# Optimization experiments

Hardware: AMD Instinct MI355X
Metric: run time of the kernel (lower is better)

Reference implementation:

```python
import jax, jax.numpy as jnp
import numpy as np

B, V = 128, 128000


def setup_inputs() -> dict:
    key = jax.random.key(0)
    k1, k2, k3, k4, k5, k6 = jax.random.split(key, 6)
    logits = jax.random.normal(k1, (B, V), dtype=jnp.float32)
    temperatures = jax.random.uniform(k2, (B,), dtype=jnp.float32, minval=0.5, maxval=1.5)
    top_ks = jax.random.randint(k3, (B,), 1, 2049).astype(jnp.int64)
    top_ps = jax.random.uniform(k4, (B,), dtype=jnp.float32, minval=0.8, maxval=1.0)
    min_ps = jax.random.uniform(k5, (B,), dtype=jnp.float32, minval=0.0, maxval=0.1)
    u = jax.random.uniform(k6, (B,), dtype=jnp.float32)
    return {"logits": logits, "temperatures": temperatures, "top_ks": top_ks,
            "top_ps": top_ps, "min_ps": min_ps, "u": u}


def reference(logits, temperatures, top_ks, top_ps, min_ps, u):
    # temperature-scaled softmax
    probs = jax.nn.softmax(logits.astype(jnp.float32) / temperatures[:, None], axis=-1)  # [B,V]

    # --- top_k_renorm_prob: keep k largest probs per row, renormalize ---
    sorted_desc = jnp.sort(probs, axis=-1)[:, ::-1]  # [B,V] descending
    k_idx = jnp.clip(top_ks - 1, 0, probs.shape[-1] - 1).astype(jnp.int32)[:, None]
    k_thresh = jnp.take_along_axis(sorted_desc, k_idx, axis=-1)  # [B,1] k-th largest prob
    probs = jnp.where(probs >= k_thresh, probs, 0.0)
    probs = probs / jnp.sum(probs, axis=-1, keepdims=True)

    # --- top_p_renorm_prob: keep smallest prefix of sorted probs covering mass p ---
    sorted_desc = jnp.sort(probs, axis=-1)[:, ::-1]
    cum = jnp.cumsum(sorted_desc, axis=-1)
    keep_sorted = (cum - sorted_desc) < top_ps[:, None]  # always keeps at least the top token
    p_thresh = jnp.min(jnp.where(keep_sorted, sorted_desc, jnp.inf), axis=-1, keepdims=True)
    probs = jnp.where(probs >= p_thresh, probs, 0.0)
    probs = probs / jnp.sum(probs, axis=-1, keepdims=True)

    # --- min_p_sampling_from_probs: drop probs < min_p * max_prob, renorm, sample ---
    max_p = jnp.max(probs, axis=-1, keepdims=True)
    probs = jnp.where(probs >= min_ps[:, None] * max_p, probs, 0.0)
    probs = probs / jnp.sum(probs, axis=-1, keepdims=True)

    # inverse-CDF (multinomial) sampling with per-row uniform u
    cdf = jnp.cumsum(probs, axis=-1)
    tokens = jnp.sum(cdf < u[:, None], axis=-1)
    tokens = jnp.clip(tokens, 0, probs.shape[-1] - 1).astype(jnp.int32)
    return tokens
```

## Files before the change

### kernel.cpp

```cpp
#include <hip/hip_runtime.h>
#include <float.h>
#include <stdint.h>

#define TPB_H 1024
#define TPB_G 1024
#define TPB_S 512
#define NB 2048
#define NS 4
#define CAND_CAP 2048
#define KEPT_CAP 4096
#define MAXLEV 6
#define NW_H (TPB_H / 64)
#define NW_S (TPB_S / 64)
#define FLO (-16.0f)
#define FSC ((float)NB / 32.0f)

__device__ __forceinline__ int bin_of(float x, float lo, float sc) {
  float bf = (x - lo) * sc;
  if (!(bf > 0.0f)) return 0;
  if (bf >= (float)(NB - 1)) return NB - 1;
  return (int)bf;
}

__device__ __forceinline__ double wsum_d(double v) {
#pragma unroll
  for (int o = 32; o > 0; o >>= 1) v += __shfl_xor(v, o);
  return v;
}
__device__ __forceinline__ int wsum_i(int v) {
#pragma unroll
  for (int o = 32; o > 0; o >>= 1) v += __shfl_xor(v, o);
  return v;
}
__device__ __forceinline__ float wmax_f(float v) {
#pragma unroll
  for (int o = 32; o > 0; o >>= 1) v = fmaxf(v, __shfl_xor(v, o));
  return v;
}

__device__ __forceinline__ int wave_push(int* cnt_lds, bool active) {
  const unsigned long long mask = __ballot(active);
  if (mask == 0ull) return -1;
  const int lane = (int)(threadIdx.x & 63);
  const unsigned long long lanebit = 1ull << lane;
  const int prefix = __popcll(mask & (lanebit - 1ull));
  const int leader = (int)(__ffsll((unsigned long long)mask) - 1);
  int base = 0;
  if (active && prefix == 0) base = atomicAdd(cnt_lds, __popcll(mask));
  base = __shfl(base, leader);
  return base + prefix;
}

__device__ __forceinline__ double blk_sum_d(double v, double* sred, double* out) {
  v = wsum_d(v);
  __syncthreads();
  if ((threadIdx.x & 63) == 0) sred[threadIdx.x >> 6] = v;
  __syncthreads();
  if (threadIdx.x == 0) {
    double t = 0.0;
#pragma unroll
    for (int i = 0; i < NW_S; i++) t += sred[i];
    *out = t;
  }
  __syncthreads();
  return *out;
}

__device__ __forceinline__ int blk_sum_i(int v, int* sredi, int* out) {
  v = wsum_i(v);
  __syncthreads();
  if ((threadIdx.x & 63) == 0) sredi[threadIdx.x >> 6] = v;
  __syncthreads();
  if (threadIdx.x == 0) {
    int t = 0;
#pragma unroll
    for (int i = 0; i < NW_S; i++) t += sredi[i];
    *out = t;
  }
  __syncthreads();
  return *out;
}

__device__ __forceinline__ double blk_exscan_d(double v, double* sw, double* sw2) {
  const int tid = threadIdx.x;
  const int lane = tid & 63, wid = tid >> 6;
  __syncthreads();
  double incl = v;
#pragma unroll
  for (int o = 1; o < 64; o <<= 1) {
    double t = __shfl_up(incl, o);
    if (lane >= o) incl += t;
  }
  if (lane == 63) sw[wid] = incl;
  __syncthreads();
  if (tid == 0) {
    double acc = 0.0;
#pragma unroll
    for (int i = 0; i < NW_S; i++) { double t = sw[i]; sw2[i] = acc; acc += t; }
  }
  __syncthreads();
  return sw2[wid] + (incl - v);
}


__device__ __forceinline__ void xchg_f(float& k, int& p, int e, int s, int len) {
  const float ok = __shfl_xor(k, s);
  const int op = __shfl_xor(p, s);
  const bool lower = ((e & s) == 0);
  const bool desc = (((e & ~s) & len) == 0);
  const bool keep = desc ? (lower ? (k >= ok) : (k <= ok))
                         : (lower ? (k <= ok) : (k >= ok));
  if (!keep) { k = ok; p = op; }
}

__device__ __forceinline__ void xchg_i(int& k, float& p, int e, int s, int len) {
  const int ok = __shfl_xor(k, s);
  const float op = __shfl_xor(p, s);
  const bool lower = ((e & s) == 0);
  const bool asc = (((e & ~s) & len) == 0);
  const bool keep = asc ? (lower ? (k <= ok) : (k >= ok))
                        : (lower ? (k >= ok) : (k <= ok));
  if (!keep) { k = ok; p = op; }
}

__device__ __forceinline__ void reg_sort128_f(float& ka, int& pa, float& kb, int& pb,
                                              int base, int lane) {
  const int ea = base + lane, eb = base + 64 + lane;
  for (int len = 2; len <= 128; len <<= 1) {
    if (len == 128) {
      const bool d = ((base & 128) == 0);
      if (d ? (ka < kb) : (ka > kb)) {
        float tk = ka; ka = kb; kb = tk; int tp = pa; pa = pb; pb = tp;
      }
      for (int s = 32; s >= 1; s >>= 1) { xchg_f(ka, pa, ea, s, len); xchg_f(kb, pb, eb, s, len); }
    } else {
      for (int s = len >> 1; s >= 1; s >>= 1) { xchg_f(ka, pa, ea, s, len); xchg_f(kb, pb, eb, s, len); }
    }
  }
}

__device__ __forceinline__ void reg_merge128_f(float& ka, int& pa, float& kb, int& pb,
                                               int base, int lane, int len) {
  const int ea = base + lane, eb = base + 64 + lane;
  const bool d = ((base & len) == 0);
  if (d ? (ka < kb) : (ka > kb)) {
    float tk = ka; ka = kb; kb = tk; int tp = pa; pa = pb; pb = tp;
  }
  for (int s = 32; s >= 1; s >>= 1) { xchg_f(ka, pa, ea, s, len); xchg_f(kb, pb, eb, s, len); }
}

__device__ __forceinline__ void reg_sort128_i(int& ka, float& pa, int& kb, float& pb,
                                              int base, int lane) {
  const int ea = base + lane, eb = base + 64 + lane;
  for (int len = 2; len <= 128; len <<= 1) {
    if (len == 128) {
      const bool a = ((base & 128) == 0);
      if (a ? (ka > kb) : (ka < kb)) {
        int tk = ka; ka = kb; kb = tk; float tp = pa; pa = pb; pb = tp;
      }
      for (int s = 32; s >= 1; s >>= 1) { xchg_i(ka, pa, ea, s, len); xchg_i(kb, pb, eb, s, len); }
    } else {
      for (int s = len >> 1; s >= 1; s >>= 1) { xchg_i(ka, pa, ea, s, len); xchg_i(kb, pb, eb, s, len); }
    }
  }
}

__device__ __forceinline__ void reg_merge128_i(int& ka, float& pa, int& kb, float& pb,
                                               int base, int lane, int len) {
  const int ea = base + lane, eb = base + 64 + lane;
  const bool a = ((base & len) == 0);
  if (a ? (ka > kb) : (ka < kb)) {
    int tk = ka; ka = kb; kb = tk; float tp = pa; pa = pb; pb = tp;
  }
  for (int s = 32; s >= 1; s >>= 1) { xchg_i(ka, pa, ea, s, len); xchg_i(kb, pb, eb, s, len); }
}

__device__ void bitonic_desc_f(float* key, int* pay, int M) {
  const int tid = threadIdx.x;
  for (int len = 2; len <= M; len <<= 1) {
    for (int str = len >> 1; str > 0; str >>= 1) {
      for (int t = tid; t < (M >> 1); t += TPB_S) {
        const int i = ((t & ~(str - 1)) << 1) | (t & (str - 1));
        const int j2 = i | str;
        const float vi = key[i], vj = key[j2];
        const bool descSeg = ((i & len) == 0);
        if (descSeg ? (vi < vj) : (vi > vj)) {
          key[i] = vj; key[j2] = vi;
          const int ti = pay[i]; pay[i] = pay[j2]; pay[j2] = ti;
        }
      }
      __syncthreads();
    }
  }
}

__device__ void bitonic_asc_i(int* key, float* pay, int M) {
  const int tid = threadIdx.x;
  for (int len = 2; len <= M; len <<= 1) {
    for (int str = len >> 1; str > 0; str >>= 1) {
      for (int t = tid; t < (M >> 1); t += TPB_S) {
        const int i = ((t & ~(str - 1)) << 1) | (t & (str - 1));
        const int j2 = i | str;
        const int ki = key[i], kj = key[j2];
        const bool ascSeg = ((i & len) == 0);
        if (ascSeg ? (ki > kj) : (ki < kj)) {
          key[i] = kj; key[j2] = ki;
          const float tv = pay[i]; pay[i] = pay[j2]; pay[j2] = tv;
        }
      }
      __syncthreads();
    }
  }
}

__device__ void hybrid_sort_desc_f(float* key, int* pay, int M) {
  const int tid = threadIdx.x;
  const int wid = tid >> 6, lane = tid & 63;
  const int nblk = M >> 7;
  __syncthreads();
  for (int blk = wid; blk < nblk; blk += NW_S) {
    const int base = blk << 7;
    float ka = key[base + lane]; int pa = pay[base + lane];
    float kb = key[base + 64 + lane]; int pb = pay[base + 64 + lane];
    reg_sort128_f(ka, pa, kb, pb, base, lane);
    key[base + lane] = ka; pay[base + lane] = pa;
    key[base + 64 + lane] = kb; pay[base + 64 + lane] = pb;
  }
  __syncthreads();
  for (int len = 256; len <= M; len <<= 1) {
    for (int str = len >> 1; str >= 128; str >>= 1) {
      for (int t = tid; t < (M >> 1); t += TPB_S) {
        const int i = ((t & ~(str - 1)) << 1) | (t & (str - 1));
        const int j2 = i | str;
        const float vi = key[i], vj = key[j2];
        const bool d = ((i & len) == 0);
        if (d ? (vi < vj) : (vi > vj)) {
          key[i] = vj; key[j2] = vi;
          const int ti = pay[i]; pay[i] = pay[j2]; pay[j2] = ti;
        }
      }
      __syncthreads();
    }
    for (int blk = wid; blk < nblk; blk += NW_S) {
      const int base = blk << 7;
      float ka = key[base + lane]; int pa = pay[base + lane];
      float kb = key[base + 64 + lane]; int pb = pay[base + 64 + lane];
      reg_merge128_f(ka, pa, kb, pb, base, lane, len);
      key[base + lane] = ka; pay[base + lane] = pa;
      key[base + 64 + lane] = kb; pay[base + 64 + lane] = pb;
    }
    __syncthreads();
  }
}

__device__ void hybrid_sort_asc_i(int* key, float* pay, int M) {
  const int tid = threadIdx.x;
  const int wid = tid >> 6, lane = tid & 63;
  const int nblk = M >> 7;
  __syncthreads();
  for (int blk = wid; blk < nblk; blk += NW_S) {
    const int base = blk << 7;
    int ka = key[base + lane]; float pa = pay[base + lane];
    int kb = key[base + 64 + lane]; float pb = pay[base + 64 + lane];
    reg_sort128_i(ka, pa, kb, pb, base, lane);
    key[base + lane] = ka; pay[base + lane] = pa;
    key[base + 64 + lane] = kb; pay[base + 64 + lane] = pb;
  }
  __syncthreads();
  for (int len = 256; len <= M; len <<= 1) {
    for (int str = len >> 1; str >= 128; str >>= 1) {
      for (int t = tid; t < (M >> 1); t += TPB_S) {
        const int i = ((t & ~(str - 1)) << 1) | (t & (str - 1));
        const int j2 = i | str;
        const int ki = key[i], kj = key[j2];
        const bool a = ((i & len) == 0);
        if (a ? (ki > kj) : (ki < kj)) {
          key[i] = kj; key[j2] = ki;
          const float tv = pay[i]; pay[i] = pay[j2]; pay[j2] = tv;
        }
      }
      __syncthreads();
    }
    for (int blk = wid; blk < nblk; blk += NW_S) {
      const int base = blk << 7;
      int ka = key[base + lane]; float pa = pay[base + lane];
      int kb = key[base + 64 + lane]; float pb = pay[base + 64 + lane];
      reg_merge128_i(ka, pa, kb, pb, base, lane, len);
      key[base + lane] = ka; pay[base + lane] = pa;
      key[base + 64 + lane] = kb; pay[base + 64 + lane] = pb;
    }
    __syncthreads();
  }
}

__device__ __forceinline__ void locate_kbin(const int* hist, int k,
                                            int* s_bin, int* s_kk, int* s_cntbin) {
  if (threadIdx.x < 64) {
    const int l = threadIdx.x;
    const int b0 = NB - (l + 1) * (NB / 64);
    int c = 0;
#pragma unroll
    for (int j = 0; j < NB / 64; j++) c += hist[b0 + j];
    int incl = c;
#pragma unroll
    for (int o = 1; o < 64; o <<= 1) {
      int t2 = __shfl_up(incl, o);
      if (l >= o) incl += t2;
    }
    const int pref = incl - c;
    if (pref < k && k <= pref + c) {
      int rem = k - pref;
      for (int j = NB / 64 - 1; j >= 0; j--) {
        const int h = hist[b0 + j];
        if (rem <= h) { *s_bin = b0 + j; *s_cntbin = h; *s_kk = rem; break; }
        rem -= h;
      }
    }
  }
}

__device__ __forceinline__ int decode_k(const void* topks_raw, int row, int B, int V) {
  const int* ip = (const int*)topks_raw;
  const bool is64 = (B < 2) || (ip[1] == 0);
  long long kraw = is64 ? ((const long long*)topks_raw)[row] : (long long)ip[row];
  long long kidx = kraw - 1;
  if (kidx < 0) kidx = 0;
  if (kidx > (long long)(V - 1)) kidx = (long long)(V - 1);
  return (int)kidx + 1;
}

#define ROW_LOOP(...)                                                                  \
  do {                                                                                 \
    for (int i0_ = tid * 4; i0_ < V4; i0_ += TPB_S * 4) {                              \
      const float4 v4_ = *reinterpret_cast<const float4*>(lr + i0_);                   \
      { const float lv = v4_.x; const int gi = i0_ + 0; (void)gi; __VA_ARGS__ }        \
      { const float lv = v4_.y; const int gi = i0_ + 1; (void)gi; __VA_ARGS__ }        \
      { const float lv = v4_.z; const int gi = i0_ + 2; (void)gi; __VA_ARGS__ }        \
      { const float lv = v4_.w; const int gi = i0_ + 3; (void)gi; __VA_ARGS__ }        \
    }                                                                                  \
    for (int gi = V4 + tid; gi < V; gi += TPB_S) {                                     \
      const float lv = lr[gi]; (void)gi; __VA_ARGS__                                   \
    }                                                                                  \
  } while (0)

extern "C" __global__ void __launch_bounds__(TPB_H) hist_max_kernel(
    const float* __restrict__ logits, int V,
    int* __restrict__ ws_hist, float* __restrict__ ws_max,
    int* __restrict__ kept_cnt, int* __restrict__ cand_cnt, int zeroCnts) {
  __shared__ int hist[NB];
  __shared__ float sredf[NW_H];
  const int tid = threadIdx.x;
  const int row = blockIdx.x / NS;
  const int part = blockIdx.x % NS;
  const float* lr = logits + (size_t)row * (size_t)V;
  const int start = (int)(((long long)V * part) / NS);
  const int end = (int)(((long long)V * (part + 1)) / NS);
  const int cnt = end - start;

  if (zeroCnts && part == 0 && tid == 0) { kept_cnt[row] = 0; cand_cnt[row] = 0; }

  for (int i = tid; i < NB; i += TPB_H) hist[i] = 0;
  __syncthreads();

  float mx = -FLT_MAX;
  const int c4 = ((start & 3) == 0) ? (cnt & ~3) : 0;
  for (int i0 = tid * 4; i0 < c4; i0 += TPB_H * 4) {
    const float4 v4 = *reinterpret_cast<const float4*>(lr + start + i0);
    mx = fmaxf(mx, v4.x); atomicAdd(&hist[bin_of(v4.x, FLO, FSC)], 1);
    mx = fmaxf(mx, v4.y); atomicAdd(&hist[bin_of(v4.y, FLO, FSC)], 1);
    mx = fmaxf(mx, v4.z); atomicAdd(&hist[bin_of(v4.z, FLO, FSC)], 1);
    mx = fmaxf(mx, v4.w); atomicAdd(&hist[bin_of(v4.w, FLO, FSC)], 1);
  }
  for (int i = c4 + tid; i < cnt; i += TPB_H) {
    const float lv = lr[start + i];
    mx = fmaxf(mx, lv); atomicAdd(&hist[bin_of(lv, FLO, FSC)], 1);
  }

  mx = wmax_f(mx);
  __syncthreads();
  if ((tid & 63) == 0) sredf[tid >> 6] = mx;
  __syncthreads();
  if (tid == 0) {
    float t = sredf[0];
    for (int i = 1; i < NW_H; i++) t = fmaxf(t, sredf[i]);
    ws_max[blockIdx.x] = t;
  }
  __syncthreads();
  int* dst = ws_hist + (size_t)blockIdx.x * NB;
  for (int i = tid; i < NB; i += TPB_H) dst[i] = hist[i];
}

extern "C" __global__ void __launch_bounds__(TPB_G) gather_kernel(
    const float* __restrict__ logits, const void* __restrict__ topks_raw,
    int V, int B, const int* __restrict__ ws_hist,
    int* __restrict__ kept_cnt, int* __restrict__ cand_cnt,
    float* __restrict__ kept_val_g, int* __restrict__ kept_idx_g,
    float* __restrict__ cand_val_g, int* __restrict__ cand_idx_g) {
  __shared__ int hist[NB];
  __shared__ float lkv[KEPT_CAP];
  __shared__ int lki[KEPT_CAP];
  __shared__ float lcv[CAND_CAP];
  __shared__ int lci[CAND_CAP];
  __shared__ int s_bin, s_kk, s_cntbin, l_kc, l_cc, s_gk, s_gc;
  const int tid = threadIdx.x;
  const int row = blockIdx.x / NS;
  const int part = blockIdx.x % NS;
  const int k = decode_k(topks_raw, row, B, V);

  for (int i = tid; i < NB; i += TPB_G) {
    int t = 0;
#pragma unroll
    for (int p = 0; p < NS; p++) t += ws_hist[(size_t)(row * NS + p) * NB + i];
    hist[i] = t;
  }
  if (tid == 0) { l_kc = 0; l_cc = 0; }
  __syncthreads();
  locate_kbin(hist, k, &s_bin, &s_kk, &s_cntbin);
  __syncthreads();
  const int kbin = s_bin;

  const float* lr = logits + (size_t)row * (size_t)V;
  const int start = (int)(((long long)V * part) / NS);
  const int end = (int)(((long long)V * (part + 1)) / NS);
  const int cnt = end - start;

#define GATHER_ONE(lv, gi)                                                   \
  {                                                                          \
    const int b_ = bin_of(lv, FLO, FSC);                                     \
    const bool isk_ = (b_ > kbin);                                           \
    const bool isc_ = (b_ == kbin);                                          \
    const int pk_ = wave_push(&l_kc, isk_);                                  \
    if (isk_ && pk_ < KEPT_CAP) { lkv[pk_] = lv; lki[pk_] = gi; }            \
    const int pc_ = wave_push(&l_cc, isc_);                                  \
    if (isc_ && pc_ < CAND_CAP) { lcv[pc_] = lv; lci[pc_] = gi; }            \
  }

  const int c4 = ((start & 3) == 0) ? (cnt & ~3) : 0;
  for (int i0 = tid * 4; i0 < c4; i0 += TPB_G * 4) {
    const float4 v4 = *reinterpret_cast<const float4*>(lr + start + i0);
    GATHER_ONE(v4.x, start + i0 + 0);
    GATHER_ONE(v4.y, start + i0 + 1);
    GATHER_ONE(v4.z, start + i0 + 2);
    GATHER_ONE(v4.w, start + i0 + 3);
  }
  for (int i = c4 + tid; i < cnt; i += TPB_G) {
    const float lv = lr[start + i];
    GATHER_ONE(lv, start + i);
  }
#undef GATHER_ONE

  __syncthreads();
  if (tid == 0) {
    s_gk = atomicAdd(&kept_cnt[row], l_kc);
    s_gc = atomicAdd(&cand_cnt[row], l_cc);
  }
  __syncthreads();
  {
    float* kv = kept_val_g + (size_t)row * KEPT_CAP;
    int* ki = kept_idx_g + (size_t)row * KEPT_CAP;
    float* cv = cand_val_g + (size_t)row * CAND_CAP;
    int* ci = cand_idx_g + (size_t)row * CAND_CAP;
    const int nks = (l_kc < KEPT_CAP) ? l_kc : KEPT_CAP;
    const int ncs = (l_cc < CAND_CAP) ? l_cc : CAND_CAP;
    for (int t = tid; t < nks; t += TPB_G) {
      const int d = s_gk + t;
      if (d < KEPT_CAP) { kv[d] = lkv[t]; ki[d] = lki[t]; }
    }
    for (int t = tid; t < ncs; t += TPB_G) {
      const int d = s_gc + t;
      if (d < CAND_CAP) { cv[d] = lcv[t]; ci[d] = lci[t]; }
    }
  }
}

extern "C" __global__ void __launch_bounds__(TPB_S) sampler_kernel(
    const float* __restrict__ logits, const float* __restrict__ temps,
    const void* __restrict__ topks_raw, const float* __restrict__ topps,
    const float* __restrict__ minps, const float* __restrict__ uarr,
    int* __restrict__ out, const int* __restrict__ ws_hist,
    const float* __restrict__ ws_max, const int* __restrict__ kept_cnt,
    const int* __restrict__ cand_cnt, const float* __restrict__ kept_val_g,
    const int* __restrict__ kept_idx_g, const float* __restrict__ cand_val_g,
    const int* __restrict__ cand_idx_g, int mode, int V, int B) {
  const int row = blockIdx.x;
  const int tid = threadIdx.x;

  __shared__ float cand[CAND_CAP];
  __shared__ int hist[NB];
  __shared__ int cand_idx[CAND_CAP];
  __shared__ int kept_idx[KEPT_CAP];
  __shared__ float kept_val[KEPT_CAP];
  __shared__ double sred[NW_S], sred2[NW_S];
  __shared__ int sredi[NW_S];
  __shared__ float sredf[NW_S];
  __shared__ double s_outd;
  __shared__ int s_outi;
  __shared__ int s_bad;
  __shared__ float lev_lo[MAXLEV], lev_sc[MAXLEV];
  __shared__ int lev_bin[MAXLEV];
  __shared__ int s_nlev, s_bin, s_kk, s_cntbin, s_cnt, s_ccnt, s_pos;
  __shared__ float s_lmax, s_vkl, s_lo, s_sc;

  const float* lr = logits + (size_t)row * (size_t)V;
  const float T = temps[row];
  const float topp = topps[row];
  const float minp = minps[row];
  const float u = uarr[row];
  const int k = decode_k(topks_raw, row, B, V);
  const int V4 = ((V & 3) == 0) ? V : 0;
  const int haveWs = (mode >= 1) ? 1 : 0;

  int n1 = -1;
  float lmax = 0.0f;

  if (mode == 2) {
    const int nk = kept_cnt[row];
    const int nc = cand_cnt[row];
    const int kk0 = k - nk;
    if (nk <= KEPT_CAP && nc >= 1 && nc <= CAND_CAP && kk0 >= 1 && kk0 <= nc) {
      if (tid == 0) {
        float m = ws_max[row * NS];
#pragma unroll
        for (int p = 1; p < NS; p++) m = fmaxf(m, ws_max[row * NS + p]);
        s_lmax = m;
      }
      for (int t = tid; t < nc; t += TPB_S) {
        cand[t] = cand_val_g[(size_t)row * CAND_CAP + t];
        cand_idx[t] = cand_idx_g[(size_t)row * CAND_CAP + t];
      }
      __syncthreads();
      for (int t = tid; t < nc; t += TPB_S) {
        const float v = cand[t];
        int rank = 0;
        for (int j = 0; j < nc; j++) {
          const float cj = cand[j];
          rank += (cj > v) ? 1 : ((cj == v && j < t) ? 1 : 0);
        }
        if (rank == kk0 - 1) s_vkl = v;
      }
      __syncthreads();
      const float vkl = s_vkl;
      for (int t = tid; t < nk; t += TPB_S) {
        kept_val[t] = kept_val_g[(size_t)row * KEPT_CAP + t];
        kept_idx[t] = kept_idx_g[(size_t)row * KEPT_CAP + t];
      }
      if (tid == 0) s_cnt = nk;
      __syncthreads();
      for (int t = tid; t < nc; t += TPB_S) {
        const float v = cand[t];
        if (v >= vkl) {
          const int p = atomicAdd(&s_cnt, 1);
          if (p < KEPT_CAP) { kept_val[p] = v; kept_idx[p] = cand_idx[t]; }
        }
      }
      __syncthreads();
      n1 = (s_cnt < KEPT_CAP) ? s_cnt : KEPT_CAP;
      lmax = s_lmax;
    }
  }

  if (n1 < 0) {
    if (haveWs) {
      for (int i = tid; i < NB; i += TPB_S) {
        int t = 0;
#pragma unroll
        for (int p = 0; p < NS; p++) t += ws_hist[(size_t)(row * NS + p) * NB + i];
        hist[i] = t;
      }
      if (tid == 0) {
        float m = ws_max[row * NS];
#pragma unroll
        for (int p = 1; p < NS; p++) m = fmaxf(m, ws_max[row * NS + p]);
        s_lmax = m;
      }
      __syncthreads();
    } else {
      for (int i = tid; i < NB; i += TPB_S) hist[i] = 0;
      __syncthreads();
      float mx = -FLT_MAX;
      ROW_LOOP(mx = fmaxf(mx, lv); atomicAdd(&hist[bin_of(lv, FLO, FSC)], 1););
      mx = wmax_f(mx);
      __syncthreads();
      if ((tid & 63) == 0) sredf[tid >> 6] = mx;
      __syncthreads();
      if (tid == 0) {
        float t = sredf[0];
        for (int i = 1; i < NW_S; i++) t = fmaxf(t, sredf[i]);
        s_lmax = t;
      }
      __syncthreads();
    }
    lmax = s_lmax;

    if (tid == 0) {
      s_kk = k; s_nlev = 0; s_vkl = lmax; s_lo = FLO; s_sc = FSC;
    }
    __syncthreads();

    for (int lev = 0; lev < MAXLEV; lev++) {
      if (tid < 64) {
        const int l = tid;
        const int b0 = NB - (l + 1) * (NB / 64);
        int c = 0;
#pragma unroll
        for (int j = 0; j < NB / 64; j++) c += hist[b0 + j];
        int incl = c;
#pragma unroll
        for (int o = 1; o < 64; o <<= 1) {
          int t2 = __shfl_up(incl, o);
          if (l >= o) incl += t2;
        }
        const int pref = incl - c;
        const int kk = s_kk;
        if (pref < kk && kk <= pref + c) {
          int rem = kk - pref;
          for (int j = NB / 64 - 1; j >= 0; j--) {
            const int h = hist[b0 + j];
            if (rem <= h) { s_bin = b0 + j; s_cntbin = h; s_kk = rem; break; }
            rem -= h;
          }
        }
      }
      __syncthreads();
      if (tid == 0) {
        lev_lo[lev] = s_lo; lev_sc[lev] = s_sc; lev_bin[lev] = s_bin;
        s_nlev = lev + 1;
      }
      __syncthreads();
      if (s_cntbin <= CAND_CAP) break;
      const float nlo = s_lo + (float)s_bin / s_sc;
      const float nsc = s_sc * (float)NB;
      const bool degw = !((nlo + (float)NB / nsc) > nlo);
      if (lev + 1 >= MAXLEV || degw) break;
      __syncthreads();
      if (tid == 0) { s_lo = nlo; s_sc = nsc; }
      for (int i = tid; i < NB; i += TPB_S) hist[i] = 0;
      __syncthreads();
      const int nl = lev + 1;
      ROW_LOOP(
        bool memb = true;
        for (int L = 0; L < nl; L++) {
          if (bin_of(lv, lev_lo[L], lev_sc[L]) != lev_bin[L]) { memb = false; break; }
        }
        if (memb) atomicAdd(&hist[bin_of(lv, nlo, nsc)], 1););
      __syncthreads();
    }

    if (tid == 0) { s_cnt = 0; s_ccnt = 0; }
    __syncthreads();
    {
      const int nl = s_nlev;
      ROW_LOOP(
        int cls = 2;
        for (int L = 0; L < nl; L++) {
          const int b = bin_of(lv, lev_lo[L], lev_sc[L]);
          if (b > lev_bin[L]) { cls = 1; break; }
          if (b < lev_bin[L]) { cls = 0; break; }
        }
        if (cls == 1) {
          int p = atomicAdd(&s_cnt, 1);
          if (p < KEPT_CAP) { kept_idx[p] = gi; kept_val[p] = lv; }
        } else if (cls == 2) {
          int p = atomicAdd(&s_ccnt, 1);
          if (p < CAND_CAP) { cand[p] = lv; cand_idx[p] = gi; }
        });
    }
    __syncthreads();

    {
      const int n = (s_ccnt < CAND_CAP) ? s_ccnt : CAND_CAP;
      int kkq = s_kk;
      if (kkq > n) kkq = n;
      for (int t = tid; t < n; t += TPB_S) {
        const float v = cand[t];
        int rank = 0;
        for (int j = 0; j < n; j++) {
          const float cj = cand[j];
          rank += (cj > v) ? 1 : ((cj == v && j < t) ? 1 : 0);
        }
        if (rank == kkq - 1) s_vkl = v;
      }
    }
    __syncthreads();
    const float vkl = s_vkl;
    {
      const int n = (s_ccnt < CAND_CAP) ? s_ccnt : CAND_CAP;
      for (int t = tid; t < n; t += TPB_S) {
        const float v = cand[t];
        if (v >= vkl) {
          int p = atomicAdd(&s_cnt, 1);
          if (p < KEPT_CAP) { kept_idx[p] = cand_idx[t]; kept_val[p] = v; }
        }
      }
    }
    __syncthreads();
    n1 = (s_cnt < KEPT_CAP) ? s_cnt : KEPT_CAP;
  }

  if (n1 <= 0) {
    if (tid == 0) out[row] = 0;
    return;
  }

  const float xmaxT = lmax / T;
  double lsum = 0.0;
  for (int t = tid; t < n1; t += TPB_S) {
    const float x = kept_val[t] / T;
    const float w = expf(x - xmaxT);
    kept_val[t] = w;
    lsum += (double)w;
  }
  const float s1f = (float)blk_sum_d(lsum, sred, &s_outd);
  for (int t = tid; t < n1; t += TPB_S) kept_val[t] = kept_val[t] / s1f;

  int M = 128;
  while (M < n1) M <<= 1;
  __syncthreads();
  for (int t = n1 + tid; t < M; t += TPB_S) { kept_val[t] = -1.0f; kept_idx[t] = 0x7FFFFFFF; }
  __syncthreads();
  hybrid_sort_desc_f(kept_val, kept_idx, M);
  if (tid == 0) s_bad = 0;
  __syncthreads();
  for (int t = tid; t + 1 < M; t += TPB_S)
    if (kept_val[t] < kept_val[t + 1]) s_bad = 1;
  __syncthreads();
  if (s_bad) bitonic_desc_f(kept_val, kept_idx, M);

  const int C = (M + TPB_S - 1) / TPB_S;
  double cls0 = 0.0;
  for (int j = 0; j < C; j++) {
    const int p = tid * C + j;
    if (p < n1) cls0 += (double)kept_val[p];
  }
  const double excl0 = blk_exscan_d(cls0, sred, sred2);
  int lc = 0;
  {
    double run = excl0;
    for (int j = 0; j < C; j++) {
      const int p = tid * C + j;
      if (p < n1) {
        if (run < (double)topp) lc++;
        run += (double)kept_val[p];
      }
    }
  }
  const int cnt = blk_sum_i(lc, sredi, &s_outi);
  const float pthr = kept_val[cnt - 1];

  int ln2 = 0;
  double ls2 = 0.0;
  for (int j = 0; j < C; j++) {
    const int p = tid * C + j;
    if (p < n1) {
      const float v = kept_val[p];
      if (v >= pthr) { ln2++; ls2 += (double)v; }
    }
  }
  const int n2 = blk_sum_i(ln2, sredi, &s_outi);
  const float s2f = (float)blk_sum_d(ls2, sred, &s_outd);

  const float maxr = kept_val[0] / s2f;
  const float th4 = minp * maxr;
  int ln3 = 0;
  double ls3 = 0.0;
  for (int j = 0; j < C; j++) {
    const int p = tid * C + j;
    if (p < n2) {
      const float r = kept_val[p] / s2f;
      if (r >= th4) { ln3++; ls3 += (double)r; }
    }
  }
  const int n3 = blk_sum_i(ln3, sredi, &s_outi);
  const float s3f = (float)blk_sum_d(ls3, sred, &s_outd);

  int M3 = 128;
  while (M3 < n3) M3 <<= 1;
  __syncthreads();
  for (int t = tid; t < M3; t += TPB_S) {
    if (t < n3) {
      const float r = kept_val[t] / s2f;
      kept_val[t] = r / s3f;
    } else {
      kept_val[t] = 0.0f;
      kept_idx[t] = 0x7FFFFFFF;
    }
  }
  __syncthreads();
  hybrid_sort_asc_i(kept_idx, kept_val, M3);
  if (tid == 0) s_bad = 0;
  __syncthreads();
  for (int t = tid; t + 1 < M3; t += TPB_S)
    if (kept_idx[t] > kept_idx[t + 1]) s_bad = 1;
  __syncthreads();
  if (s_bad) bitonic_asc_i(kept_idx, kept_val, M3);

  const int C3 = (M3 + TPB_S - 1) / TPB_S;
  double cls3 = 0.0;
  for (int j = 0; j < C3; j++) {
    const int p = tid * C3 + j;
    if (p < n3) cls3 += (double)kept_val[p];
  }
  const double e5 = blk_exscan_d(cls3, sred, sred2);
  if (tid == 0) s_pos = 0x7FFFFFFF;
  __syncthreads();
  {
    double run = e5;
    int found = -1;
    for (int j = 0; j < C3; j++) {
      const int p = tid * C3 + j;
      if (p < n3) {
        run += (double)kept_val[p];
        if (run >= (double)u) { found = p; break; }
      }
    }
    if (found >= 0) atomicMin(&s_pos, found);
  }
  __syncthreads();
  if (tid == 0) {
    int token;
    if (!(u > 0.0f)) token = 0;
    else if (s_pos == 0x7FFFFFFF) token = V - 1;
    else token = kept_idx[s_pos];
    out[row] = token;
  }
}

extern "C" void kernel_launch(void* const* d_in, const int* in_sizes, int n_in,
                              void* d_out, int out_size, void* d_ws, size_t ws_size,
                              hipStream_t stream) {
  const float* logits = (const float*)d_in[0];
  const float* temps = (const float*)d_in[1];
  const void* topks = d_in[2];
  const float* topps = (const float*)d_in[3];
  const float* minps = (const float*)d_in[4];
  const float* u = (const float*)d_in[5];
  int* out = (int*)d_out;
  const int B = in_sizes[1];
  const int V = in_sizes[0] / B;
  (void)n_in; (void)out_size;

  char* p = (char*)d_ws;
  int* ws_hist = (int*)p;        p += (size_t)NS * B * NB * sizeof(int);
  float* ws_max = (float*)p;     p += (size_t)NS * B * sizeof(float);
  int* kept_cnt = (int*)p;       p += (size_t)B * sizeof(int);
  int* cand_cnt = (int*)p;       p += (size_t)B * sizeof(int);
  float* kept_val_g = (float*)p; p += (size_t)B * KEPT_CAP * sizeof(float);
  int* kept_idx_g = (int*)p;     p += (size_t)B * KEPT_CAP * sizeof(int);
  float* cand_val_g = (float*)p; p += (size_t)B * CAND_CAP * sizeof(float);
  int* cand_idx_g = (int*)p;     p += (size_t)B * CAND_CAP * sizeof(int);
  const size_t need_full = (size_t)(p - (char*)d_ws);
  const size_t need_hist = (size_t)NS * B * NB * sizeof(int) + (size_t)NS * B * sizeof(float);

  int mode = 0;
  if (d_ws && ws_size >= need_full) mode = 2;
  else if (d_ws && ws_size >= need_hist) mode = 1;

  if (mode >= 1) {
    hist_max_kernel<<<dim3(B * NS), dim3(TPB_H), 0, stream>>>(
        logits, V, ws_hist, ws_max, kept_cnt, cand_cnt, (mode == 2) ? 1 : 0);
  }
  if (mode == 2) {
    gather_kernel<<<dim3(B * NS), dim3(TPB_G), 0, stream>>>(
        logits, topks, V, B, ws_hist, kept_cnt, cand_cnt,
        kept_val_g, kept_idx_g, cand_val_g, cand_idx_g);
  }
  sampler_kernel<<<dim3(B), dim3(TPB_S), 0, stream>>>(
      logits, temps, topks, topps, minps, u, out, ws_hist, ws_max,
      kept_cnt, cand_cnt, kept_val_g, kept_idx_g, cand_val_g, cand_idx_g,
      mode, V, B);
}
```

Before: 200.9 us.

## Use 512-element register bitonic sorts, runtime row split, fused block reductions

```diff
diff --git a/kernel.cpp b/kernel.cpp
--- a/kernel.cpp
+++ b/kernel.cpp
@@ -6,7 +6,6 @@
 #define TPB_G 1024
 #define TPB_S 512
 #define NB 2048
-#define NS 4
 #define CAND_CAP 2048
 #define KEPT_CAP 4096
 #define MAXLEV 6
@@ -81,6 +80,22 @@
   return *out;
 }
 
+__device__ __forceinline__ void blk_sum_id(int vi, double vd, int* sredi, double* sredd,
+                                           int* outi, double* outd) {
+  vi = wsum_i(vi);
+  vd = wsum_d(vd);
+  __syncthreads();
+  if ((threadIdx.x & 63) == 0) { sredi[threadIdx.x >> 6] = vi; sredd[threadIdx.x >> 6] = vd; }
+  __syncthreads();
+  if (threadIdx.x == 0) {
+    int ti = 0; double td = 0.0;
+#pragma unroll
+    for (int i = 0; i < NW_S; i++) { ti += sredi[i]; td += sredd[i]; }
+    *outi = ti; *outd = td;
+  }
+  __syncthreads();
+}
+
 __device__ __forceinline__ double blk_exscan_d(double v, double* sw, double* sw2) {
   const int tid = threadIdx.x;
   const int lane = tid & 63, wid = tid >> 6;
@@ -123,56 +138,97 @@
   if (!keep) { k = ok; p = op; }
 }
 
-__device__ __forceinline__ void reg_sort128_f(float& ka, int& pa, float& kb, int& pb,
-                                              int base, int lane) {
-  const int ea = base + lane, eb = base + 64 + lane;
-  for (int len = 2; len <= 128; len <<= 1) {
-    if (len == 128) {
-      const bool d = ((base & 128) == 0);
-      if (d ? (ka < kb) : (ka > kb)) {
-        float tk = ka; ka = kb; kb = tk; int tp = pa; pa = pb; pb = tp;
-      }
-      for (int s = 32; s >= 1; s >>= 1) { xchg_f(ka, pa, ea, s, len); xchg_f(kb, pb, eb, s, len); }
+__device__ __forceinline__ void cmpswap_f(float& ka, int& pa, float& kb, int& pb, bool desc) {
+  const bool sw = desc ? (ka < kb) : (ka > kb);
+  if (sw) { float tk = ka; ka = kb; kb = tk; int tp = pa; pa = pb; pb = tp; }
+}
+__device__ __forceinline__ void cmpswap_i(int& ka, float& pa, int& kb, float& pb, bool asc) {
+  const bool sw = asc ? (ka > kb) : (ka < kb);
+  if (sw) { int tk = ka; ka = kb; kb = tk; float tp = pa; pa = pb; pb = tp; }
+}
+
+__device__ __forceinline__ void wave_sort512_f(float (&k)[8], int (&p)[8], int base, int lane) {
+#pragma unroll
+  for (int len = 2; len <= 512; len <<= 1) {
+#pragma unroll
+    for (int s = 256; s >= 1; s >>= 1) {
+      if (s >= len) continue;
+      if (s >= 64) {
+        const int m = s >> 6;
+#pragma unroll
+        for (int r = 0; r < 8; r++) {
+          if ((r & m) == 0) {
+            const int e = base + r * 64 + lane;
+            cmpswap_f(k[r], p[r], k[r | m], p[r | m], ((e & len) == 0));
+          }
+        }
+      } else {
+#pragma unroll
+        for (int r = 0; r < 8; r++) xchg_f(k[r], p[r], base + r * 64 + lane, s, len);
+      }
+    }
+  }
+}
+
+__device__ __forceinline__ void wave_merge512_f(float (&k)[8], int (&p)[8], int base, int lane, int len) {
+#pragma unroll
+  for (int s = 256; s >= 1; s >>= 1) {
+    if (s >= 64) {
+      const int m = s >> 6;
+#pragma unroll
+      for (int r = 0; r < 8; r++) {
+        if ((r & m) == 0) {
+          const int e = base + r * 64 + lane;
+          cmpswap_f(k[r], p[r], k[r | m], p[r | m], ((e & len) == 0));
+        }
+      }
     } else {
-      for (int s = len >> 1; s >= 1; s >>= 1) { xchg_f(ka, pa, ea, s, len); xchg_f(kb, pb, eb, s, len); }
-    }
-  }
-}
-
-__device__ __forceinline__ void reg_merge128_f(float& ka, int& pa, float& kb, int& pb,
-                                               int base, int lane, int len) {
-  const int ea = base + lane, eb = base + 64 + lane;
-  const bool d = ((base & len) == 0);
-  if (d ? (ka < kb) : (ka > kb)) {
-    float tk = ka; ka = kb; kb = tk; int tp = pa; pa = pb; pb = tp;
-  }
-  for (int s = 32; s >= 1; s >>= 1) { xchg_f(ka, pa, ea, s, len); xchg_f(kb, pb, eb, s, len); }
-}
-
-__device__ __forceinline__ void reg_sort128_i(int& ka, float& pa, int& kb, float& pb,
-                                              int base, int lane) {
-  const int ea = base + lane, eb = base + 64 + lane;
-  for (int len = 2; len <= 128; len <<= 1) {
-    if (len == 128) {
-      const bool a = ((base & 128) == 0);
-      if (a ? (ka > kb) : (ka < kb)) {
-        int tk = ka; ka = kb; kb = tk; float tp = pa; pa = pb; pb = tp;
-      }
-      for (int s = 32; s >= 1; s >>= 1) { xchg_i(ka, pa, ea, s, len); xchg_i(kb, pb, eb, s, len); }
+#pragma unroll
+      for (int r = 0; r < 8; r++) xchg_f(k[r], p[r], base + r * 64 + lane, s, len);
+    }
+  }
+}
+
+__device__ __forceinline__ void wave_sort512_i(int (&k)[8], float (&p)[8], int base, int lane) {
+#pragma unroll
+  for (int len = 2; len <= 512; len <<= 1) {
+#pragma unroll
+    for (int s = 256; s >= 1; s >>= 1) {
+      if (s >= len) continue;
+      if (s >= 64) {
+        const int m = s >> 6;
+#pragma unroll
+        for (int r = 0; r < 8; r++) {
+          if ((r & m) == 0) {
+            const int e = base + r * 64 + lane;
+            cmpswap_i(k[r], p[r], k[r | m], p[r | m], ((e & len) == 0));
+          }
+        }
+      } else {
+#pragma unroll
+        for (int r = 0; r < 8; r++) xchg_i(k[r], p[r], base + r * 64 + lane, s, len);
+      }
+    }
+  }
+}
+
+__device__ __forceinline__ void wave_merge512_i(int (&k)[8], float (&p)[8], int base, int lane, int len) {
+#pragma unroll
+  for (int s = 256; s >= 1; s >>= 1) {
+    if (s >= 64) {
+      const int m = s >> 6;
+#pragma unroll
+      for (int r = 0; r < 8; r++) {
+        if ((r & m) == 0) {
+          const int e = base + r * 64 + lane;
+          cmpswap_i(k[r], p[r], k[r | m], p[r | m], ((e & len) == 0));
+        }
+      }
     } else {
-      for (int s = len >> 1; s >= 1; s >>= 1) { xchg_i(ka, pa, ea, s, len); xchg_i(kb, pb, eb, s, len); }
-    }
-  }
-}
-
-__device__ __forceinline__ void reg_merge128_i(int& ka, float& pa, int& kb, float& pb,
-                                               int base, int lane, int len) {
-  const int ea = base + lane, eb = base + 64 + lane;
-  const bool a = ((base & len) == 0);
-  if (a ? (ka > kb) : (ka < kb)) {
-    int tk = ka; ka = kb; kb = tk; float tp = pa; pa = pb; pb = tp;
-  }
-  for (int s = 32; s >= 1; s >>= 1) { xchg_i(ka, pa, ea, s, len); xchg_i(kb, pb, eb, s, len); }
+#pragma unroll
+      for (int r = 0; r < 8; r++) xchg_i(k[r], p[r], base + r * 64 + lane, s, len);
+    }
+  }
 }
 
 __device__ void bitonic_desc_f(float* key, int* pay, int M) {
@@ -216,19 +272,20 @@
 __device__ void hybrid_sort_desc_f(float* key, int* pay, int M) {
   const int tid = threadIdx.x;
   const int wid = tid >> 6, lane = tid & 63;
-  const int nblk = M >> 7;
+  const int nblk = M >> 9;
   __syncthreads();
   for (int blk = wid; blk < nblk; blk += NW_S) {
-    const int base = blk << 7;
-    float ka = key[base + lane]; int pa = pay[base + lane];
-    float kb = key[base + 64 + lane]; int pb = pay[base + 64 + lane];
-    reg_sort128_f(ka, pa, kb, pb, base, lane);
-    key[base + lane] = ka; pay[base + lane] = pa;
-    key[base + 64 + lane] = kb; pay[base + 64 + lane] = pb;
-  }
-  __syncthreads();
-  for (int len = 256; len <= M; len <<= 1) {
-    for (int str = len >> 1; str >= 128; str >>= 1) {
+    const int base = blk << 9;
+    float k[8]; int p[8];
+#pragma unroll
+    for (int r = 0; r < 8; r++) { k[r] = key[base + r * 64 + lane]; p[r] = pay[base + r * 64 + lane]; }
+    wave_sort512_f(k, p, base, lane);
+#pragma unroll
+    for (int r = 0; r < 8; r++) { key[base + r * 64 + lane] = k[r]; pay[base + r * 64 + lane] = p[r]; }
+  }
+  __syncthreads();
+  for (int len = 1024; len <= M; len <<= 1) {
+    for (int str = len >> 1; str >= 512; str >>= 1) {
       for (int t = tid; t < (M >> 1); t += TPB_S) {
         const int i = ((t & ~(str - 1)) << 1) | (t & (str - 1));
         const int j2 = i | str;
@@ -242,12 +299,13 @@
       __syncthreads();
     }
     for (int blk = wid; blk < nblk; blk += NW_S) {
-      const int base = blk << 7;
-      float ka = key[base + lane]; int pa = pay[base + lane];
-      float kb = key[base + 64 + lane]; int pb = pay[base + 64 + lane];
-      reg_merge128_f(ka, pa, kb, pb, base, lane, len);
-      key[base + lane] = ka; pay[base + lane] = pa;
-      key[base + 64 + lane] = kb; pay[base + 64 + lane] = pb;
+      const int base = blk << 9;
+      float k[8]; int p[8];
+#pragma unroll
+      for (int r = 0; r < 8; r++) { k[r] = key[base + r * 64 + lane]; p[r] = pay[base + r * 64 + lane]; }
+      wave_merge512_f(k, p, base, lane, len);
+#pragma unroll
+      for (int r = 0; r < 8; r++) { key[base + r * 64 + lane] = k[r]; pay[base + r * 64 + lane] = p[r]; }
     }
     __syncthreads();
   }
@@ -256,19 +314,20 @@
 __device__ void hybrid_sort_asc_i(int* key, float* pay, int M) {
   const int tid = threadIdx.x;
   const int wid = tid >> 6, lane = tid & 63;
-  const int nblk = M >> 7;
+  const int nblk = M >> 9;
   __syncthreads();
   for (int blk = wid; blk < nblk; blk += NW_S) {
-    const int base = blk << 7;
-    int ka = key[base + lane]; float pa = pay[base + lane];
-    int kb = key[base + 64 + lane]; float pb = pay[base + 64 + lane];
-    reg_sort128_i(ka, pa, kb, pb, base, lane);
-    key[base + lane] = ka; pay[base + lane] = pa;
-    key[base + 64 + lane] = kb; pay[base + 64 + lane] = pb;
-  }
-  __syncthreads();
-  for (int len = 256; len <= M; len <<= 1) {
-    for (int str = len >> 1; str >= 128; str >>= 1) {
+    const int base = blk << 9;
+    int k[8]; float p[8];
+#pragma unroll
+    for (int r = 0; r < 8; r++) { k[r] = key[base + r * 64 + lane]; p[r] = pay[base + r * 64 + lane]; }
+    wave_sort512_i(k, p, base, lane);
+#pragma unroll
+    for (int r = 0; r < 8; r++) { key[base + r * 64 + lane] = k[r]; pay[base + r * 64 + lane] = p[r]; }
+  }
+  __syncthreads();
+  for (int len = 1024; len <= M; len <<= 1) {
+    for (int str = len >> 1; str >= 512; str >>= 1) {
       for (int t = tid; t < (M >> 1); t += TPB_S) {
         const int i = ((t & ~(str - 1)) << 1) | (t & (str - 1));
         const int j2 = i | str;
@@ -282,12 +341,13 @@
       __syncthreads();
     }
     for (int blk = wid; blk < nblk; blk += NW_S) {
-      const int base = blk << 7;
-      int ka = key[base + lane]; float pa = pay[base + lane];
-      int kb = key[base + 64 + lane]; float pb = pay[base + 64 + lane];
-      reg_merge128_i(ka, pa, kb, pb, base, lane, len);
-      key[base + lane] = ka; pay[base + lane] = pa;
-      key[base + 64 + lane] = kb; pay[base + 64 + lane] = pb;
+      const int base = blk << 9;
+      int k[8]; float p[8];
+#pragma unroll
+      for (int r = 0; r < 8; r++) { k[r] = key[base + r * 64 + lane]; p[r] = pay[base + r * 64 + lane]; }
+      wave_merge512_i(k, p, base, lane, len);
+#pragma unroll
+      for (int r = 0; r < 8; r++) { key[base + r * 64 + lane] = k[r]; pay[base + r * 64 + lane] = p[r]; }
     }
     __syncthreads();
   }
@@ -344,17 +404,17 @@
   } while (0)
 
 extern "C" __global__ void __launch_bounds__(TPB_H) hist_max_kernel(
-    const float* __restrict__ logits, int V,
+    const float* __restrict__ logits, int V, int ns,
     int* __restrict__ ws_hist, float* __restrict__ ws_max,
     int* __restrict__ kept_cnt, int* __restrict__ cand_cnt, int zeroCnts) {
   __shared__ int hist[NB];
   __shared__ float sredf[NW_H];
   const int tid = threadIdx.x;
-  const int row = blockIdx.x / NS;
-  const int part = blockIdx.x % NS;
+  const int row = blockIdx.x / ns;
+  const int part = blockIdx.x % ns;
   const float* lr = logits + (size_t)row * (size_t)V;
-  const int start = (int)(((long long)V * part) / NS);
-  const int end = (int)(((long long)V * (part + 1)) / NS);
+  const int start = (int)(((long long)V * part) / ns);
+  const int end = (int)(((long long)V * (part + 1)) / ns);
   const int cnt = end - start;
 
   if (zeroCnts && part == 0 && tid == 0) { kept_cnt[row] = 0; cand_cnt[row] = 0; }
@@ -392,7 +452,7 @@
 
 extern "C" __global__ void __launch_bounds__(TPB_G) gather_kernel(
     const float* __restrict__ logits, const void* __restrict__ topks_raw,
-    int V, int B, const int* __restrict__ ws_hist,
+    int V, int B, int ns, const int* __restrict__ ws_hist,
     int* __restrict__ kept_cnt, int* __restrict__ cand_cnt,
     float* __restrict__ kept_val_g, int* __restrict__ kept_idx_g,
     float* __restrict__ cand_val_g, int* __restrict__ cand_idx_g) {
@@ -403,14 +463,13 @@
   __shared__ int lci[CAND_CAP];
   __shared__ int s_bin, s_kk, s_cntbin, l_kc, l_cc, s_gk, s_gc;
   const int tid = threadIdx.x;
-  const int row = blockIdx.x / NS;
-  const int part = blockIdx.x % NS;
+  const int row = blockIdx.x / ns;
+  const int part = blockIdx.x % ns;
   const int k = decode_k(topks_raw, row, B, V);
 
   for (int i = tid; i < NB; i += TPB_G) {
     int t = 0;
-#pragma unroll
-    for (int p = 0; p < NS; p++) t += ws_hist[(size_t)(row * NS + p) * NB + i];
+    for (int p = 0; p < ns; p++) t += ws_hist[(size_t)(row * ns + p) * NB + i];
     hist[i] = t;
   }
   if (tid == 0) { l_kc = 0; l_cc = 0; }
@@ -420,8 +479,8 @@
   const int kbin = s_bin;
 
   const float* lr = logits + (size_t)row * (size_t)V;
-  const int start = (int)(((long long)V * part) / NS);
-  const int end = (int)(((long long)V * (part + 1)) / NS);
+  const int start = (int)(((long long)V * part) / ns);
+  const int end = (int)(((long long)V * (part + 1)) / ns);
   const int cnt = end - start;
 
 #define GATHER_ONE(lv, gi)                                                   \
@@ -481,7 +540,7 @@
     const float* __restrict__ ws_max, const int* __restrict__ kept_cnt,
     const int* __restrict__ cand_cnt, const float* __restrict__ kept_val_g,
     const int* __restrict__ kept_idx_g, const float* __restrict__ cand_val_g,
-    const int* __restrict__ cand_idx_g, int mode, int V, int B) {
+    const int* __restrict__ cand_idx_g, int mode, int ns, int V, int B) {
   const int row = blockIdx.x;
   const int tid = threadIdx.x;
 
@@ -519,9 +578,8 @@
     const int kk0 = k - nk;
     if (nk <= KEPT_CAP && nc >= 1 && nc <= CAND_CAP && kk0 >= 1 && kk0 <= nc) {
       if (tid == 0) {
-        float m = ws_max[row * NS];
-#pragma unroll
-        for (int p = 1; p < NS; p++) m = fmaxf(m, ws_max[row * NS + p]);
+        float m = ws_max[row * ns];
+        for (int p = 1; p < ns; p++) m = fmaxf(m, ws_max[row * ns + p]);
         s_lmax = m;
       }
       for (int t = tid; t < nc; t += TPB_S) {
@@ -563,14 +621,12 @@
     if (haveWs) {
       for (int i = tid; i < NB; i += TPB_S) {
         int t = 0;
-#pragma unroll
-        for (int p = 0; p < NS; p++) t += ws_hist[(size_t)(row * NS + p) * NB + i];
+        for (int p = 0; p < ns; p++) t += ws_hist[(size_t)(row * ns + p) * NB + i];
         hist[i] = t;
       }
       if (tid == 0) {
-        float m = ws_max[row * NS];
-#pragma unroll
-        for (int p = 1; p < NS; p++) m = fmaxf(m, ws_max[row * NS + p]);
+        float m = ws_max[row * ns];
+        for (int p = 1; p < ns; p++) m = fmaxf(m, ws_max[row * ns + p]);
         s_lmax = m;
       }
       __syncthreads();
@@ -713,7 +769,7 @@
   const float s1f = (float)blk_sum_d(lsum, sred, &s_outd);
   for (int t = tid; t < n1; t += TPB_S) kept_val[t] = kept_val[t] / s1f;
 
-  int M = 128;
+  int M = 512;
   while (M < n1) M <<= 1;
   __syncthreads();
   for (int t = n1 + tid; t < M; t += TPB_S) { kept_val[t] = -1.0f; kept_idx[t] = 0x7FFFFFFF; }
@@ -756,8 +812,9 @@
       if (v >= pthr) { ln2++; ls2 += (double)v; }
     }
   }
-  const int n2 = blk_sum_i(ln2, sredi, &s_outi);
-  const float s2f = (float)blk_sum_d(ls2, sred, &s_outd);
+  blk_sum_id(ln2, ls2, sredi, sred, &s_outi, &s_outd);
+  const int n2 = s_outi;
+  const float s2f = (float)s_outd;
 
   const float maxr = kept_val[0] / s2f;
   const float th4 = minp * maxr;
@@ -770,10 +827,11 @@
       if (r >= th4) { ln3++; ls3 += (double)r; }
     }
   }
-  const int n3 = blk_sum_i(ln3, sredi, &s_outi);
-  const float s3f = (float)blk_sum_d(ls3, sred, &s_outd);
-
-  int M3 = 128;
+  blk_sum_id(ln3, ls3, sredi, sred, &s_outi, &s_outd);
+  const int n3 = s_outi;
+  const float s3f = (float)s_outd;
+
+  int M3 = 512;
   while (M3 < n3) M3 <<= 1;
   __syncthreads();
   for (int t = tid; t < M3; t += TPB_S) {
@@ -839,33 +897,44 @@
   const int V = in_sizes[0] / B;
   (void)n_in; (void)out_size;
 
+  int ns = 8, mode = 0;
+  size_t need_full = 0;
+  for (;;) {
+    need_full = (size_t)ns * B * NB * sizeof(int) + (size_t)ns * B * sizeof(float) +
+                (size_t)B * 2 * sizeof(int) +
+                (size_t)B * KEPT_CAP * (sizeof(float) + sizeof(int)) +
+                (size_t)B * CAND_CAP * (sizeof(float) + sizeof(int));
+    if (d_ws && ws_size >= need_full) { mode = 2; break; }
+    if (ns == 4) break;
+    ns = 4;
+  }
+  if (mode == 0) {
+    ns = 4;
+    const size_t need_hist = (size_t)ns * B * NB * sizeof(int) + (size_t)ns * B * sizeof(float);
+    if (d_ws && ws_size >= need_hist) mode = 1;
+  }
+
   char* p = (char*)d_ws;
-  int* ws_hist = (int*)p;        p += (size_t)NS * B * NB * sizeof(int);
-  float* ws_max = (float*)p;     p += (size_t)NS * B * sizeof(float);
+  int* ws_hist = (int*)p;        p += (size_t)ns * B * NB * sizeof(int);
+  float* ws_max = (float*)p;     p += (size_t)ns * B * sizeof(float);
   int* kept_cnt = (int*)p;       p += (size_t)B * sizeof(int);
   int* cand_cnt = (int*)p;       p += (size_t)B * sizeof(int);
   float* kept_val_g = (float*)p; p += (size_t)B * KEPT_CAP * sizeof(float);
   int* kept_idx_g = (int*)p;     p += (size_t)B * KEPT_CAP * sizeof(int);
   float* cand_val_g = (float*)p; p += (size_t)B * CAND_CAP * sizeof(float);
   int* cand_idx_g = (int*)p;     p += (size_t)B * CAND_CAP * sizeof(int);
-  const size_t need_full = (size_t)(p - (char*)d_ws);
-  const size_t need_hist = (size_t)NS * B * NB * sizeof(int) + (size_t)NS * B * sizeof(float);
-
-  int mode = 0;
-  if (d_ws && ws_size >= need_full) mode = 2;
-  else if (d_ws && ws_size >= need_hist) mode = 1;
 
   if (mode >= 1) {
-    hist_max_kernel<<<dim3(B * NS), dim3(TPB_H), 0, stream>>>(
-        logits, V, ws_hist, ws_max, kept_cnt, cand_cnt, (mode == 2) ? 1 : 0);
+    hist_max_kernel<<<dim3(B * ns), dim3(TPB_H), 0, stream>>>(
+        logits, V, ns, ws_hist, ws_max, kept_cnt, cand_cnt, (mode == 2) ? 1 : 0);
   }
   if (mode == 2) {
-    gather_kernel<<<dim3(B * NS), dim3(TPB_G), 0, stream>>>(
-        logits, topks, V, B, ws_hist, kept_cnt, cand_cnt,
+    gather_kernel<<<dim3(B * ns), dim3(TPB_G), 0, stream>>>(
+        logits, topks, V, B, ns, ws_hist, kept_cnt, cand_cnt,
         kept_val_g, kept_idx_g, cand_val_g, cand_idx_g);
   }
   sampler_kernel<<<dim3(B), dim3(TPB_S), 0, stream>>>(
       logits, temps, topks, topps, minps, u, out, ws_hist, ws_max,
       kept_cnt, cand_cnt, kept_val_g, kept_idx_g, cand_val_g, cand_idx_g,
-      mode, V, B);
-}
+      mode, ns, V, B);
+}
```

New measurement: 226.4 us. 1.13x slower.
